# Optimization experiments

Hardware: AMD Instinct MI355X
Metric: run time of the kernel (lower is better)

Reference implementation:

```python
import jax, jax.numpy as jnp
import numpy as np

B, LQ, LK, F = 8, 4096, 4096, 64


def setup_inputs() -> dict:
    key = jax.random.key(0)
    ks = jax.random.split(key, 9)
    s = 1.0 / np.sqrt(F)
    return {
        "query": jax.random.normal(ks[0], (B, LQ, F), dtype=jnp.float32),
        "key": jax.random.normal(ks[1], (B, LK, F), dtype=jnp.float32),
        "value": jax.random.normal(ks[2], (B, LQ, F), dtype=jnp.float32),
        "wq": jax.random.normal(ks[3], (F, F), dtype=jnp.float32) * s,
        "bq": jax.random.normal(ks[4], (F,), dtype=jnp.float32) * 0.01,
        "wk": jax.random.normal(ks[5], (F, F), dtype=jnp.float32) * s,
        "bk": jax.random.normal(ks[6], (F,), dtype=jnp.float32) * 0.01,
        "wv": jax.random.normal(ks[7], (F, F), dtype=jnp.float32) * s,
        "bv": jax.random.normal(ks[8], (F,), dtype=jnp.float32) * 0.01,
    }


def reference(query, key, value, wq, bq, wk, bk, wv, bv):
    # nn.Linear: x @ W.T + b
    q = query @ wq.T + bq          # [B, LQ, F]
    k = key @ wk.T + bk            # [B, LK, F]
    v = value @ wv.T + bv          # [B, LQ, F]
    # scores[b, i, j] = <k_i, q_j>; NO 1/sqrt(d) scaling (faithful to source)
    scores = jnp.einsum('bkf,bqf->bkq', k, q)       # [B, LK, LQ]
    attn = jax.nn.softmax(scores, axis=-1)          # softmax over query positions
    return jnp.einsum('bkq,bqf->bkf', attn, v)      # [B, LK, F]
```

## Files before the change

kernel.cpp:

```cpp
#include <hip/hip_runtime.h>


typedef unsigned short u16;
typedef __attribute__((ext_vector_type(4))) unsigned int u32x4;
typedef __attribute__((ext_vector_type(4))) float f32x4;
typedef __attribute__((ext_vector_type(16))) float f32x16;
typedef __attribute__((ext_vector_type(2))) float f32x2;
typedef __attribute__((ext_vector_type(8))) short s16x8;

#define MFMA32(a, bb, c) __builtin_amdgcn_mfma_f32_32x32x16_bf16((a), (bb), (c), 0, 0, 0)
#define MFMA16(a, bb, c) __builtin_amdgcn_mfma_f32_16x16x32_bf16((a), (bb), (c), 0, 0, 0)

#if __has_builtin(__builtin_amdgcn_exp2f)
#define FEXP2(x) __builtin_amdgcn_exp2f(x)
#else
#define FEXP2(x) exp2f(x)
#endif

__device__ __forceinline__ short f2bf(float x) {
    unsigned u = __builtin_bit_cast(unsigned, x);
    u += 0x7fffu + ((u >> 16) & 1u);
    return (short)(u >> 16);
}
__device__ __forceinline__ float bf2f(short h) {
    unsigned u = ((unsigned)(u16)h) << 16;
    return __builtin_bit_cast(float, u);
}
__device__ __forceinline__ f32x4 zero4() { f32x4 r = {0.f, 0.f, 0.f, 0.f}; return r; }

__device__ __forceinline__ unsigned pktrunc(float lo, float hi) {
#if __has_builtin(__builtin_amdgcn_perm)
    return __builtin_amdgcn_perm(__builtin_bit_cast(unsigned, hi),
                                 __builtin_bit_cast(unsigned, lo), 0x07060302u);
#else
    return (__builtin_bit_cast(unsigned, hi) & 0xffff0000u)
         | (__builtin_bit_cast(unsigned, lo) >> 16);
#endif
}

__device__ __forceinline__ void split8(f32x4 a, f32x4 b, s16x8& hi, s16x8& lo) {
#pragma unroll
    for (int i = 0; i < 4; i++) {
        short h = f2bf(a[i]);
        hi[i] = h;
        lo[i] = f2bf(a[i] - bf2f(h));
    }
#pragma unroll
    for (int i = 0; i < 4; i++) {
        short h = f2bf(b[i]);
        hi[i + 4] = h;
        lo[i + 4] = f2bf(b[i] - bf2f(h));
    }
}

__global__ __launch_bounds__(256) void proj_qkv_32727650796335(
    const float* __restrict__ q_, const float* __restrict__ k_, const float* __restrict__ v_,
    const float* __restrict__ wq, const float* __restrict__ bq,
    const float* __restrict__ wk, const float* __restrict__ bk,
    const float* __restrict__ wv, const float* __restrict__ bv,
    u16* __restrict__ qp, u16* __restrict__ kph, u16* __restrict__ kpl,
    u16* __restrict__ vp) {
    const int z = blockIdx.y;
    const float* X  = (z == 0) ? q_ : (z == 1) ? k_ : v_;
    const float* W  = (z == 0) ? wq : (z == 1) ? wk : wv;
    const float* bi = (z == 0) ? bq : (z == 1) ? bk : bv;

    const int t = threadIdx.x;
    const int w = t >> 6, ln = t & 63, g = ln >> 4, lq = ln & 15;
    const int cidx = blockIdx.x;

    __shared__ f32x4 ldsX[1024];
    __shared__ __align__(16) u16 outH[4096];
    __shared__ __align__(16) u16 outLo[4096];

    const f32x4* X4 = (const f32x4*)X + (size_t)cidx * 1024;
#pragma unroll
    for (int kk = 0; kk < 4; kk++) {
        int lin = t + 256 * kk;
        int r = lin >> 4, c4 = lin & 15;
        ldsX[r * 16 + (c4 ^ (r & 7))] = X4[lin];
    }
    __syncthreads();

    float bv4[4];
#pragma unroll
    for (int nt = 0; nt < 4; nt++) bv4[nt] = bi[lq + 16 * nt];

    const f32x4* W4 = (const f32x4*)W;
    s16x8 wfh[4][2], wfl[4][2];
#pragma unroll
    for (int nt = 0; nt < 4; nt++)
#pragma unroll
        for (int kb = 0; kb < 2; kb++) {
            f32x4 a = W4[(lq + 16 * nt) * 16 + (g + 8 * kb)];
            f32x4 b = W4[(lq + 16 * nt) * 16 + (g + 4 + 8 * kb)];
            split8(a, b, wfh[nt][kb], wfl[nt][kb]);
        }

    s16x8 afh[2], afl[2];
#pragma unroll
    for (int kb = 0; kb < 2; kb++) {
        f32x4 a = ldsX[(16 * w + lq) * 16 + ((g + 8 * kb) ^ (lq & 7))];
        f32x4 b = ldsX[(16 * w + lq) * 16 + ((g + 4 + 8 * kb) ^ (lq & 7))];
        split8(a, b, afh[kb], afl[kb]);
    }

    f32x4 acc[4];
#pragma unroll
    for (int nt = 0; nt < 4; nt++) acc[nt] = zero4();
#pragma unroll
    for (int kb = 0; kb < 2; kb++)
#pragma unroll
        for (int nt = 0; nt < 4; nt++) {
            acc[nt] = MFMA16(afh[kb], wfh[nt][kb], acc[nt]);
            acc[nt] = MFMA16(afh[kb], wfl[nt][kb], acc[nt]);
            acc[nt] = MFMA16(afl[kb], wfh[nt][kb], acc[nt]);
        }

#pragma unroll
    for (int nt = 0; nt < 4; nt++)
#pragma unroll
        for (int r = 0; r < 4; r++) {
            float val = acc[nt][r] + bv4[nt];
            if (z == 1) val *= 1.44269504f;
            short hi = f2bf(val);
            int row = 16 * w + 4 * g + r;
            int f = lq + 16 * nt;
            unsigned idx;
            if (z == 0) {
                idx = (unsigned)((row >> 5) * 2048 + nt * 512
                    + ((row & 31) + ((lq >> 3) & 1) * 32) * 8 + (lq & 7));
            } else if (z == 1) {
                idx = (unsigned)(row * 64 + f);
            } else {
                idx = (unsigned)((f >> 5) * 2048 + (row >> 4) * 512
                    + ((f & 31) + ((row >> 2) & 1) * 32) * 8
                    + ((row >> 3) & 1) * 4 + (row & 3));
            }
            outH[idx] = (u16)hi;
            if (z == 1) outLo[idx] = (u16)f2bf(val - bf2f(hi));
        }
    __syncthreads();

    u16* dH = (z == 0) ? qp : (z == 1) ? kph : vp;
    u32x4* d4 = (u32x4*)(dH + (size_t)cidx * 4096);
    const u32x4* sH = (const u32x4*)outH;
    d4[t] = sH[t];
    d4[t + 256] = sH[t + 256];
    if (z == 1) {
        u32x4* d4l = (u32x4*)(kpl + (size_t)cidx * 4096);
        const u32x4* sL = (const u32x4*)outLo;
        d4l[t] = sL[t];
        d4l[t + 256] = sL[t + 256];
    }
}

__global__ __launch_bounds__(256, 4) void attn_fwd_32727650796335(
    const u16* __restrict__ qp, const u16* __restrict__ kph,
    const u16* __restrict__ kpl, const u16* __restrict__ vp,
    float* __restrict__ out, float* __restrict__ pO, f32x2* __restrict__ pML,
    int nsplit) {
    const int t = threadIdx.x;
    const int w = t >> 6, ln = t & 63, i5 = ln & 31, h = ln >> 5;
    const int itile = blockIdx.x, b = blockIdx.y, split = blockIdx.z;
    const int nc = 64 / nsplit;
    const int c0 = split * nc;

    __shared__ u32x4 ldsbuf[2][1024];

    const int irow = b * 4096 + itile * 128 + 32 * w + i5;
    const u16* krh = kph + (size_t)irow * 64;
    const u16* krl = kpl + (size_t)irow * 64;
    s16x8 kfh[4], kfl[4];
#pragma unroll
    for (int ks = 0; ks < 4; ks++) {
        kfh[ks] = *(const s16x8*)(krh + 16 * ks + 8 * h);
        kfl[ks] = *(const s16x8*)(krl + 16 * ks + 8 * h);
    }

    f32x16 oacc0 = {}, oacc1 = {};
    float m = -__builtin_inff();
    float lsum = 0.f;

    const u32x4* qsrc = (const u32x4*)(qp + (size_t)(b * 64) * 4096);
    const u32x4* vsrc = (const u32x4*)(vp + (size_t)(b * 64) * 4096);

    u32x4 qa, qb, va, vb;
#define LOADC(c) do { size_t o_ = (size_t)(c) * 512 + t;      \
        qa = qsrc[o_]; qb = qsrc[o_ + 256];                   \
        va = vsrc[o_]; vb = vsrc[o_ + 256]; } while (0)

    LOADC(c0);
    ldsbuf[0][t] = qa;
    ldsbuf[0][t + 256] = qb;
    ldsbuf[0][t + 512] = va;
    ldsbuf[0][t + 768] = vb;

    int cur = 0;
    for (int cc = 0; cc < nc; cc++) {
        __syncthreads();
        if (cc + 1 < nc) LOADC(c0 + cc + 1);
        const char* ldsc = (const char*)ldsbuf[cur];

        f32x16 s0 = {}, s1 = {};
        __builtin_amdgcn_s_setprio(1);
#pragma unroll
        for (int ks = 0; ks < 4; ks++) {
            const int fo = ks * 1024 + ln * 16;
            s16x8 q0 = *(const s16x8*)(ldsc + fo);
            s16x8 q1 = *(const s16x8*)(ldsc + 4096 + fo);
            s0 = MFMA32(q0, kfh[ks], s0);
            s1 = MFMA32(q1, kfh[ks], s1);
            s0 = MFMA32(q0, kfl[ks], s0);
            s1 = MFMA32(q1, kfl[ks], s1);
        }
        __builtin_amdgcn_s_setprio(0);

        float mx[11];
#pragma unroll
        for (int r = 0; r < 10; r++)
            mx[r] = fmaxf(fmaxf((r < 8 ? s0[2 * r] : s1[2 * (r - 8)]),
                                (r < 8 ? s0[2 * r + 1] : s1[2 * (r - 8) + 1])),
                          (r < 8 ? (r < 5 ? s1[r + 6] : s0[r + 11])
                                 : s1[2 * (r - 8) + 4]));
        mx[10] = fmaxf(s1[2], s1[3]);
        float a0 = fmaxf(fmaxf(mx[0], mx[1]), mx[2]);
        float a1 = fmaxf(fmaxf(mx[3], mx[4]), mx[5]);
        float a2 = fmaxf(fmaxf(mx[6], mx[7]), mx[8]);
        float a3 = fmaxf(mx[9], mx[10]);
        float pmax = fmaxf(fmaxf(a0, a1), fmaxf(a2, a3));
        pmax = fmaxf(pmax, __shfl_xor(pmax, 32));

        if (!__all(pmax <= m + 8.f)) {
            float mnew = fmaxf(m, pmax);
            float corr = FEXP2(m - mnew);
            lsum *= corr;
#pragma unroll
            for (int r = 0; r < 16; r++) { oacc0[r] *= corr; oacc1[r] *= corr; }
            m = mnew;
        }

        float psum = 0.f;
#pragma unroll
        for (int r = 0; r < 16; r++) {
            s0[r] = FEXP2(s0[r] - m);
            s1[r] = FEXP2(s1[r] - m);
            psum += s0[r] + s1[r];
        }
        psum += __shfl_xor(psum, 32);
        lsum += psum;

        s16x8 pf[4];
#pragma unroll
        for (int qh = 0; qh < 2; qh++) {
            u32x4 pa, pb;
#pragma unroll
            for (int r = 0; r < 4; r++) {
                pa[r] = pktrunc(s0[8 * qh + 2 * r], s0[8 * qh + 2 * r + 1]);
                pb[r] = pktrunc(s1[8 * qh + 2 * r], s1[8 * qh + 2 * r + 1]);
            }
            pf[qh]     = __builtin_bit_cast(s16x8, pa);
            pf[2 + qh] = __builtin_bit_cast(s16x8, pb);
        }

        __builtin_amdgcn_s_setprio(1);
#pragma unroll
        for (int s4 = 0; s4 < 4; s4++) {
            s16x8 vf0 = *(const s16x8*)(ldsc + 8192 + s4 * 1024 + ln * 16);
            s16x8 vf1 = *(const s16x8*)(ldsc + 12288 + s4 * 1024 + ln * 16);
            oacc0 = MFMA32(vf0, pf[s4], oacc0);
            oacc1 = MFMA32(vf1, pf[s4], oacc1);
        }
        __builtin_amdgcn_s_setprio(0);

        if (cc + 1 < nc) {
            ldsbuf[cur ^ 1][t] = qa;
            ldsbuf[cur ^ 1][t + 256] = qb;
            ldsbuf[cur ^ 1][t + 512] = va;
            ldsbuf[cur ^ 1][t + 768] = vb;
        }
        cur ^= 1;
    }
#undef LOADC

    if (nsplit == 1) {
        float inv = 1.f / lsum;
#pragma unroll
        for (int q = 0; q < 4; q++) {
            f32x4 o0, o1;
#pragma unroll
            for (int r = 0; r < 4; r++) {
                o0[r] = oacc0[4 * q + r] * inv;
                o1[r] = oacc1[4 * q + r] * inv;
            }
            *(f32x4*)(out + (size_t)irow * 64 + 8 * q + 4 * h) = o0;
            *(f32x4*)(out + (size_t)irow * 64 + 32 + 8 * q + 4 * h) = o1;
        }
    } else {
        size_t base = ((size_t)split * 32768 + (size_t)irow) * 64;
#pragma unroll
        for (int q = 0; q < 4; q++) {
            f32x4 o0, o1;
#pragma unroll
            for (int r = 0; r < 4; r++) {
                o0[r] = oacc0[4 * q + r];
                o1[r] = oacc1[4 * q + r];
            }
            *(f32x4*)(pO + base + 8 * q + 4 * h) = o0;
            *(f32x4*)(pO + base + 32 + 8 * q + 4 * h) = o1;
        }
        if (ln < 32) {
            f32x2 ml; ml[0] = m; ml[1] = lsum;
            pML[(size_t)split * 32768 + irow] = ml;
        }
    }
}

__global__ __launch_bounds__(256) void combine_32727650796335(
    const float* __restrict__ pO, const f32x2* __restrict__ pML,
    float* __restrict__ out, int nsplit) {
    const int bt = blockIdx.x;
    const int t = threadIdx.x;
    const int row = t >> 2, fb = (t & 3) << 4;
    const size_t grow = (size_t)bt * 64 + row;

    float M = -__builtin_inff();
#pragma unroll
    for (int s = 0; s < 4; s++)
        if (s < nsplit) M = fmaxf(M, pML[(size_t)s * 32768 + grow][0]);

    float wgt[4];
    float W = 0.f;
#pragma unroll
    for (int s = 0; s < 4; s++) {
        if (s < nsplit) {
            f32x2 ml = pML[(size_t)s * 32768 + grow];
            wgt[s] = exp2f(ml[0] - M);
            W += wgt[s] * ml[1];
        } else wgt[s] = 0.f;
    }
    float inv = 1.f / W;

#pragma unroll
    for (int ff = 0; ff < 16; ff += 4) {
        f32x4 acc = zero4();
#pragma unroll
        for (int s = 0; s < 4; s++)
            if (s < nsplit)
                acc += wgt[s] * *(const f32x4*)(pO + ((size_t)s * 32768 + grow) * 64 + fb + ff);
        *(f32x4*)(out + grow * 64 + fb + ff) = acc * inv;
    }
}

extern "C" void kernel_launch(void* const* d_in, const int* in_sizes, int n_in,
                              void* d_out, int out_size, void* d_ws, size_t ws_size,
                              hipStream_t stream) {
    (void)in_sizes; (void)n_in; (void)out_size;
    const float* q_ = (const float*)d_in[0];
    const float* k_ = (const float*)d_in[1];
    const float* v_ = (const float*)d_in[2];
    const float* wq = (const float*)d_in[3];
    const float* bq = (const float*)d_in[4];
    const float* wk = (const float*)d_in[5];
    const float* bk = (const float*)d_in[6];
    const float* wv = (const float*)d_in[7];
    const float* bv = (const float*)d_in[8];

    const size_t PLANE = (size_t)8 * 4096 * 64;
    u16* qp  = (u16*)d_ws;
    u16* kph = qp + PLANE;
    u16* kpl = kph + PLANE;
    u16* vp  = kpl + PLANE;
    const size_t planes_bytes = 4 * PLANE * sizeof(u16);

    auto fits = [&](int js) {
        size_t need = planes_bytes
                    + (size_t)js * 32768 * 64 * sizeof(float)
                    + (size_t)js * 32768 * sizeof(f32x2);
        return need <= ws_size;
    };
    int nsplit = fits(4) ? 4 : (fits(2) ? 2 : 1);

    float* pO  = (float*)((char*)d_ws + planes_bytes);
    f32x2* pML = (f32x2*)((char*)d_ws + planes_bytes
                          + (size_t)nsplit * 32768 * 64 * sizeof(float));

    proj_qkv_32727650796335<<<dim3(512, 3, 1), 256, 0, stream>>>(
        q_, k_, v_, wq, bq, wk, bk, wv, bv, qp, kph, kpl, vp);
    attn_fwd_32727650796335<<<dim3(32, 8, nsplit), 256, 0, stream>>>(
        qp, kph, kpl, vp, (float*)d_out, pO, pML, nsplit);
    if (nsplit > 1)
        combine_32727650796335<<<dim3(512, 1, 1), 256, 0, stream>>>(
            pO, pML, (float*)d_out, nsplit);
}
```

Baseline: 112.2 us.

## Stream Q/V fragments directly from global memory and precompute split weight fragments

The attention kernel drops its LDS double buffer and barriers, with each wave loading Q and V fragments straight from global memory (relying on L2/L1 reuse across waves). Blocks shrink to 128 threads covering 64 rows, and a flattened grid puts the batch index in the low bits so neighbouring blocks share the same Q/V. A new tiny kernel converts the weights to hi/lo bf16 fragments once, so projection blocks stop repeating the split. This trades explicit LDS staging for more global and cache traffic per wave and adds an extra kernel launch.

```diff
diff --git a/kernel.cpp b/kernel.cpp
--- a/kernel.cpp
+++ b/kernel.cpp
@@ -53,16 +53,35 @@
     }
 }
 
+__global__ __launch_bounds__(256) void prep_w_32727650796335(
+    const float* __restrict__ wq, const float* __restrict__ wk,
+    const float* __restrict__ wv, u32x4* __restrict__ whl) {
+    const int z = blockIdx.x;
+    const float* W = (z == 0) ? wq : (z == 1) ? wk : wv;
+    const f32x4* W4 = (const f32x4*)W;
+#pragma unroll
+    for (int it = 0; it < 2; it++) {
+        int unit = threadIdx.x + 256 * it;
+        int nt = unit >> 7, kb = (unit >> 6) & 1, ln = unit & 63;
+        int g = ln >> 4, lq = ln & 15;
+        f32x4 a = W4[(lq + 16 * nt) * 16 + (g + 8 * kb)];
+        f32x4 b = W4[(lq + 16 * nt) * 16 + (g + 4 + 8 * kb)];
+        s16x8 hi, lo;
+        split8(a, b, hi, lo);
+        int slot = (z * 8 + nt * 2 + kb) * 64 + ln;
+        whl[slot] = __builtin_bit_cast(u32x4, hi);
+        whl[slot + 1536] = __builtin_bit_cast(u32x4, lo);
+    }
+}
+
 __global__ __launch_bounds__(256) void proj_qkv_32727650796335(
     const float* __restrict__ q_, const float* __restrict__ k_, const float* __restrict__ v_,
-    const float* __restrict__ wq, const float* __restrict__ bq,
-    const float* __restrict__ wk, const float* __restrict__ bk,
-    const float* __restrict__ wv, const float* __restrict__ bv,
+    const float* __restrict__ bq, const float* __restrict__ bk, const float* __restrict__ bv,
+    const u32x4* __restrict__ whl,
     u16* __restrict__ qp, u16* __restrict__ kph, u16* __restrict__ kpl,
     u16* __restrict__ vp) {
     const int z = blockIdx.y;
     const float* X  = (z == 0) ? q_ : (z == 1) ? k_ : v_;
-    const float* W  = (z == 0) ? wq : (z == 1) ? wk : wv;
     const float* bi = (z == 0) ? bq : (z == 1) ? bk : bv;
 
     const int t = threadIdx.x;
@@ -86,15 +105,14 @@
 #pragma unroll
     for (int nt = 0; nt < 4; nt++) bv4[nt] = bi[lq + 16 * nt];
 
-    const f32x4* W4 = (const f32x4*)W;
     s16x8 wfh[4][2], wfl[4][2];
 #pragma unroll
     for (int nt = 0; nt < 4; nt++)
 #pragma unroll
         for (int kb = 0; kb < 2; kb++) {
-            f32x4 a = W4[(lq + 16 * nt) * 16 + (g + 8 * kb)];
-            f32x4 b = W4[(lq + 16 * nt) * 16 + (g + 4 + 8 * kb)];
-            split8(a, b, wfh[nt][kb], wfl[nt][kb]);
+            int slot = (z * 8 + nt * 2 + kb) * 64 + ln;
+            wfh[nt][kb] = __builtin_bit_cast(s16x8, whl[slot]);
+            wfl[nt][kb] = __builtin_bit_cast(s16x8, whl[slot + 1536]);
         }
 
     s16x8 afh[2], afl[2];
@@ -155,20 +173,22 @@
     }
 }
 
-__global__ __launch_bounds__(256, 4) void attn_fwd_32727650796335(
+__global__ __launch_bounds__(128, 3) void attn_fwd_32727650796335(
     const u16* __restrict__ qp, const u16* __restrict__ kph,
     const u16* __restrict__ kpl, const u16* __restrict__ vp,
     float* __restrict__ out, float* __restrict__ pO, f32x2* __restrict__ pML,
     int nsplit) {
-    const int t = threadIdx.x;
-    const int w = t >> 6, ln = t & 63, i5 = ln & 31, h = ln >> 5;
-    const int itile = blockIdx.x, b = blockIdx.y, split = blockIdx.z;
+    const int flat = blockIdx.x;
+    const int b = flat & 7;
+    const int rest = flat >> 3;
+    const int itile = rest & 63;
+    const int split = rest >> 6;
+    const int wv = threadIdx.x >> 6, ln = threadIdx.x & 63;
+    const int i5 = ln & 31, h = ln >> 5;
     const int nc = 64 / nsplit;
     const int c0 = split * nc;
 
-    __shared__ u32x4 ldsbuf[2][1024];
-
-    const int irow = b * 4096 + itile * 128 + 32 * w + i5;
+    const int irow = b * 4096 + itile * 64 + 32 * wv + i5;
     const u16* krh = kph + (size_t)irow * 64;
     const u16* krl = kpl + (size_t)irow * 64;
     s16x8 kfh[4], kfl[4];
@@ -185,36 +205,31 @@
     const u32x4* qsrc = (const u32x4*)(qp + (size_t)(b * 64) * 4096);
     const u32x4* vsrc = (const u32x4*)(vp + (size_t)(b * 64) * 4096);
 
-    u32x4 qa, qb, va, vb;
-#define LOADC(c) do { size_t o_ = (size_t)(c) * 512 + t;      \
-        qa = qsrc[o_]; qb = qsrc[o_ + 256];                   \
-        va = vsrc[o_]; vb = vsrc[o_ + 256]; } while (0)
-
-    LOADC(c0);
-    ldsbuf[0][t] = qa;
-    ldsbuf[0][t + 256] = qb;
-    ldsbuf[0][t + 512] = va;
-    ldsbuf[0][t + 768] = vb;
-
-    int cur = 0;
     for (int cc = 0; cc < nc; cc++) {
-        __syncthreads();
-        if (cc + 1 < nc) LOADC(c0 + cc + 1);
-        const char* ldsc = (const char*)ldsbuf[cur];
+        const u32x4* qc = qsrc + (size_t)(c0 + cc) * 512 + ln;
+        const u32x4* vc = vsrc + (size_t)(c0 + cc) * 512 + ln;
+
+        u32x4 q00 = qc[0],   q01 = qc[64],  q02 = qc[128], q03 = qc[192];
+        u32x4 q10 = qc[256], q11 = qc[320], q12 = qc[384], q13 = qc[448];
 
         f32x16 s0 = {}, s1 = {};
         __builtin_amdgcn_s_setprio(1);
-#pragma unroll
-        for (int ks = 0; ks < 4; ks++) {
-            const int fo = ks * 1024 + ln * 16;
-            s16x8 q0 = *(const s16x8*)(ldsc + fo);
-            s16x8 q1 = *(const s16x8*)(ldsc + 4096 + fo);
-            s0 = MFMA32(q0, kfh[ks], s0);
-            s1 = MFMA32(q1, kfh[ks], s1);
-            s0 = MFMA32(q0, kfl[ks], s0);
-            s1 = MFMA32(q1, kfl[ks], s1);
-        }
+#define QKS(qa_, qb_, ks_) do {                                         \
+        s16x8 q0_ = __builtin_bit_cast(s16x8, qa_);                     \
+        s16x8 q1_ = __builtin_bit_cast(s16x8, qb_);                     \
+        s0 = MFMA32(q0_, kfh[ks_], s0);                                 \
+        s1 = MFMA32(q1_, kfh[ks_], s1);                                 \
+        s0 = MFMA32(q0_, kfl[ks_], s0);                                 \
+        s1 = MFMA32(q1_, kfl[ks_], s1); } while (0)
+        QKS(q00, q10, 0);
+        QKS(q01, q11, 1);
+        QKS(q02, q12, 2);
+        QKS(q03, q13, 3);
+#undef QKS
         __builtin_amdgcn_s_setprio(0);
+
+        u32x4 v00 = vc[0],   v01 = vc[64],  v02 = vc[128], v03 = vc[192];
+        u32x4 v10 = vc[256], v11 = vc[320], v12 = vc[384], v13 = vc[448];
 
         float mx[11];
 #pragma unroll
@@ -264,24 +279,16 @@
         }
 
         __builtin_amdgcn_s_setprio(1);
-#pragma unroll
-        for (int s4 = 0; s4 < 4; s4++) {
-            s16x8 vf0 = *(const s16x8*)(ldsc + 8192 + s4 * 1024 + ln * 16);
-            s16x8 vf1 = *(const s16x8*)(ldsc + 12288 + s4 * 1024 + ln * 16);
-            oacc0 = MFMA32(vf0, pf[s4], oacc0);
-            oacc1 = MFMA32(vf1, pf[s4], oacc1);
-        }
+#define PVS(va_, vb_, s4_) do {                                         \
+        oacc0 = MFMA32(__builtin_bit_cast(s16x8, va_), pf[s4_], oacc0); \
+        oacc1 = MFMA32(__builtin_bit_cast(s16x8, vb_), pf[s4_], oacc1); } while (0)
+        PVS(v00, v10, 0);
+        PVS(v01, v11, 1);
+        PVS(v02, v12, 2);
+        PVS(v03, v13, 3);
+#undef PVS
         __builtin_amdgcn_s_setprio(0);
-
-        if (cc + 1 < nc) {
-            ldsbuf[cur ^ 1][t] = qa;
-            ldsbuf[cur ^ 1][t + 256] = qb;
-            ldsbuf[cur ^ 1][t + 512] = va;
-            ldsbuf[cur ^ 1][t + 768] = vb;
-        }
-        cur ^= 1;
-    }
-#undef LOADC
+    }
 
     if (nsplit == 1) {
         float inv = 1.f / lsum;
@@ -372,22 +379,25 @@
     u16* kpl = kph + PLANE;
     u16* vp  = kpl + PLANE;
     const size_t planes_bytes = 4 * PLANE * sizeof(u16);
+    u32x4* whl = (u32x4*)((char*)d_ws + planes_bytes);
+    const size_t whl_bytes = 3072 * sizeof(u32x4);
 
     auto fits = [&](int js) {
-        size_t need = planes_bytes
+        size_t need = planes_bytes + whl_bytes
                     + (size_t)js * 32768 * 64 * sizeof(float)
                     + (size_t)js * 32768 * sizeof(f32x2);
         return need <= ws_size;
     };
     int nsplit = fits(4) ? 4 : (fits(2) ? 2 : 1);
 
-    float* pO  = (float*)((char*)d_ws + planes_bytes);
-    f32x2* pML = (f32x2*)((char*)d_ws + planes_bytes
+    float* pO  = (float*)((char*)d_ws + planes_bytes + whl_bytes);
+    f32x2* pML = (f32x2*)((char*)d_ws + planes_bytes + whl_bytes
                           + (size_t)nsplit * 32768 * 64 * sizeof(float));
 
+    prep_w_32727650796335<<<dim3(3, 1, 1), 256, 0, stream>>>(wq, wk, wv, whl);
     proj_qkv_32727650796335<<<dim3(512, 3, 1), 256, 0, stream>>>(
-        q_, k_, v_, wq, bq, wk, bk, wv, bv, qp, kph, kpl, vp);
-    attn_fwd_32727650796335<<<dim3(32, 8, nsplit), 256, 0, stream>>>(
+        q_, k_, v_, bq, bk, bv, whl, qp, kph, kpl, vp);
+    attn_fwd_32727650796335<<<dim3(8 * 64 * nsplit, 1, 1), 128, 0, stream>>>(
         qp, kph, kpl, vp, (float*)d_out, pO, pML, nsplit);
     if (nsplit > 1)
         combine_32727650796335<<<dim3(512, 1, 1), 256, 0, stream>>>(
```

New measurement: 112.5 us. No clear change (+0.3%).
